# Kernel tuning notes

Measured on AMD Instinct MI355X. Metric: run time of the kernel, lower is better.

The kernel has to match this reference:

```python
import jax, jax.numpy as jnp
import numpy as np

IN_CH = 512
MAX_MID = 512


def setup_inputs() -> dict:
    key = jax.random.key(0)
    k0, k1, k2, k3, k4 = jax.random.split(key, 5)
    B, C, H, W = 32, IN_CH, 64, 64
    x = jax.random.normal(k0, (B, C, H, W), dtype=jnp.float32)
    # torch.nn.Linear params: weight [out, in], bias [out]
    s1 = 1.0 / np.sqrt(C)
    w1 = jax.random.uniform(k1, (MAX_MID * 2, C), minval=-s1, maxval=s1, dtype=jnp.float32)
    b1 = jax.random.uniform(k2, (MAX_MID * 2,), minval=-s1, maxval=s1, dtype=jnp.float32)
    s2 = 1.0 / np.sqrt(MAX_MID * 2)
    w2 = jax.random.uniform(k3, (MAX_MID, MAX_MID * 2), minval=-s2, maxval=s2, dtype=jnp.float32)
    b2 = jax.random.uniform(k4, (MAX_MID,), minval=-s2, maxval=s2, dtype=jnp.float32)
    return {"x": x, "w1": w1, "b1": b1, "w2": w2, "b2": b2}


def reference(x, w1, b1, w2, b2):
    # Global average pool: [B, C, H, W] -> [B, C]
    gap = jnp.mean(x, axis=(2, 3))
    # Tiny 2-layer MLP: Linear -> ReLU -> Linear -> Sigmoid
    h = jax.nn.relu(gap @ w1.T + b1)
    scores = jax.nn.sigmoid(h @ w2.T + b2)  # [B, MAX_MID]
    B, M = scores.shape
    # Eval path: scale from mean score, clamped
    scale = jnp.clip(jnp.mean(scores), 0.25, 1.0)
    k_min = max(4, M // 4)
    k = jnp.clip(jnp.ceil(M * scale).astype(jnp.int32), k_min, M)  # scalar int
    # topk mask with dynamic k but static shapes: threshold = k-th largest per row
    sorted_desc = jnp.sort(scores, axis=1)[:, ::-1]  # [B, M] descending
    idx = jnp.full((B, 1), k - 1, dtype=jnp.int32)
    thresh = jnp.take_along_axis(sorted_desc, idx, axis=1)  # [B, 1]
    mask = (scores >= thresh).astype(scores.dtype)  # [B, M]
    return mask[:, :, None, None], k
```

## Files before the change

### kernel.cpp

```cpp
#include <hip/hip_runtime.h>

#define NB    32
#define CIN   512
#define MID2  1024
#define MID   512
#define HW    4096

typedef float f32x4 __attribute__((ext_vector_type(4)));

__global__ __launch_bounds__(256, 8) void k_gap(const float* __restrict__ x,
                                                float* __restrict__ gap) {
    const int r0 = blockIdx.x * 2;
    const int t  = threadIdx.x;
    const f32x4* p0 = (const f32x4*)(x + (size_t)r0 * HW);
    const f32x4* p1 = (const f32x4*)(x + (size_t)(r0 + 1) * HW);
    float a0 = 0.f, a1 = 0.f;
#pragma unroll
    for (int i = 0; i < 4; ++i) {
        f32x4 u = __builtin_nontemporal_load(&p0[i * 256 + t]);
        f32x4 v = __builtin_nontemporal_load(&p1[i * 256 + t]);
        a0 += (u.x + u.y) + (u.z + u.w);
        a1 += (v.x + v.y) + (v.z + v.w);
    }
    for (int off = 32; off; off >>= 1) {
        a0 += __shfl_down(a0, off, 64);
        a1 += __shfl_down(a1, off, 64);
    }
    __shared__ float w0[4], w1[4];
    const int wid = t >> 6, lane = t & 63;
    if (lane == 0) { w0[wid] = a0; w1[wid] = a1; }
    __syncthreads();
    if (t == 0) gap[r0]     = ((w0[0] + w0[1]) + (w0[2] + w0[3])) * (1.0f / HW);
    if (t == 1) gap[r0 + 1] = ((w1[0] + w1[1]) + (w1[2] + w1[3])) * (1.0f / HW);
}

__global__ __launch_bounds__(256) void k_fc1(const float* __restrict__ gap,
                                             const float* __restrict__ w1,
                                             const float* __restrict__ b1,
                                             float* __restrict__ h) {
    const int wid = threadIdx.x >> 6, lane = threadIdx.x & 63;
    const int o4 = (blockIdx.x * 4 + wid) * 4;
    const int b  = o4 >> 10;
    const int j0 = o4 & (MID2 - 1);
    const float* g = gap + b * CIN + lane * 8;
    const float4 g0 = *(const float4*)g;
    const float4 g1 = *(const float4*)(g + 4);
    float s[4];
#pragma unroll
    for (int r = 0; r < 4; ++r) {
        const float* w = w1 + (size_t)(j0 + r) * CIN + lane * 8;
        const float4 a = *(const float4*)w;
        const float4 c = *(const float4*)(w + 4);
        s[r] = (a.x * g0.x + a.y * g0.y) + (a.z * g0.z + a.w * g0.w) +
               (c.x * g1.x + c.y * g1.y) + (c.z * g1.z + c.w * g1.w);
    }
#pragma unroll
    for (int r = 0; r < 4; ++r)
        for (int off = 32; off; off >>= 1) s[r] += __shfl_down(s[r], off, 64);
    if (lane == 0) {
#pragma unroll
        for (int r = 0; r < 4; ++r) h[o4 + r] = fmaxf(s[r] + b1[j0 + r], 0.f);
    }
}

__global__ __launch_bounds__(256) void k_fc2(const float* __restrict__ h,
                                             const float* __restrict__ w2,
                                             const float* __restrict__ b2,
                                             float* __restrict__ scores) {
    const int wid = threadIdx.x >> 6, lane = threadIdx.x & 63;
    const int o4 = (blockIdx.x * 4 + wid) * 4;
    const int b  = o4 >> 9;
    const int m0 = o4 & (MID - 1);
    const float4* h4 = (const float4*)(h + b * MID2 + lane * 16);
    const float4 h0 = h4[0], h1 = h4[1], h2 = h4[2], h3 = h4[3];
    float s[4];
#pragma unroll
    for (int r = 0; r < 4; ++r) {
        const float4* w = (const float4*)(w2 + (size_t)(m0 + r) * MID2 + lane * 16);
        const float4 a = w[0], c = w[1], d = w[2], e = w[3];
        s[r] = (a.x * h0.x + a.y * h0.y) + (a.z * h0.z + a.w * h0.w) +
               (c.x * h1.x + c.y * h1.y) + (c.z * h1.z + c.w * h1.w) +
               (d.x * h2.x + d.y * h2.y) + (d.z * h2.z + d.w * h2.w) +
               (e.x * h3.x + e.y * h3.y) + (e.z * h3.z + e.w * h3.w);
    }
#pragma unroll
    for (int r = 0; r < 4; ++r)
        for (int off = 32; off; off >>= 1) s[r] += __shfl_down(s[r], off, 64);
    if (lane == 0) {
#pragma unroll
        for (int r = 0; r < 4; ++r) {
            const float v = s[r] + b2[m0 + r];
            scores[o4 + r] = 1.0f / (1.0f + __expf(-v));
        }
    }
}

__global__ __launch_bounds__(512) void k_mask(const float* __restrict__ scores,
                                              float* __restrict__ out) {
    __shared__ float srow[MID];
    __shared__ float red[8];
    __shared__ float thr;
    const int b = blockIdx.x, t = threadIdx.x;

    float s = 0.f;
#pragma unroll
    for (int i = 0; i < NB * MID / 512; ++i) s += scores[i * 512 + t];
    for (int off = 32; off; off >>= 1) s += __shfl_down(s, off, 64);
    const int wid = t >> 6, lane = t & 63;
    if (lane == 0) red[wid] = s;

    const float v = scores[b * MID + t];
    srow[t] = v;
    __syncthreads();

    const float tot = ((red[0] + red[1]) + (red[2] + red[3])) +
                      ((red[4] + red[5]) + (red[6] + red[7]));
    const float mean = tot / (float)(NB * MID);
    const float scale = fminf(fmaxf(mean, 0.25f), 1.0f);
    int k = (int)ceilf((float)MID * scale);
    k = min(max(k, 128), MID);

    const float4* srow4 = (const float4*)srow;
    int gt = 0, ge = 0;
    for (int i = 0; i < MID / 4; ++i) {
        const float4 u = srow4[i];
        gt += (u.x > v) + (u.y > v) + (u.z > v) + (u.w > v);
        ge += (u.x >= v) + (u.y >= v) + (u.z >= v) + (u.w >= v);
    }
    if (gt < k && ge >= k) thr = v;
    __syncthreads();
    out[b * MID + t] = (v >= thr) ? 1.0f : 0.0f;
    if (b == 0 && t == 0) out[NB * MID] = (float)k;
}

extern "C" void kernel_launch(void* const* d_in, const int* in_sizes, int n_in,
                              void* d_out, int out_size, void* d_ws, size_t ws_size,
                              hipStream_t stream) {
    const float* x  = (const float*)d_in[0];
    const float* w1 = (const float*)d_in[1];
    const float* b1 = (const float*)d_in[2];
    const float* w2 = (const float*)d_in[3];
    const float* b2 = (const float*)d_in[4];
    float* out = (float*)d_out;

    float* gap    = (float*)d_ws;
    float* h      = gap + NB * CIN;
    float* scores = h + NB * MID2;

    k_gap <<<NB * CIN / 2,       256, 0, stream>>>(x, gap);
    k_fc1 <<<NB * MID2 / (4*4),  256, 0, stream>>>(gap, w1, b1, h);
    k_fc2 <<<NB * MID  / (4*4),  256, 0, stream>>>(h, w2, b2, scores);
    k_mask<<<NB,                 512, 0, stream>>>(scores, out);
}
```

Before: 67.33 us.

## Fuse GAP, two FC layers and top-k mask into one cooperative kernel

Replaces the four separate launches with a single cooperative kernel of 512 blocks that uses grid-wide syncs between the pooling, FC1, FC2 and mask phases. Each warp now pools 8 rows and computes more outputs per FC phase. This removes kernel launch gaps and tail effects, but the pooling phase, which streams a 256 MB input and dominates the work, now runs on fewer resident waves (512 blocks, launch bounds of 4 blocks per CU), which may lower memory-level parallelism. Host attribute and occupancy queries are added on every call, and the old four-kernel path is kept as a fallback.

```diff
diff --git a/kernel.cpp b/kernel.cpp
--- a/kernel.cpp
+++ b/kernel.cpp
@@ -1,4 +1,7 @@
 #include <hip/hip_runtime.h>
+#include <hip/hip_cooperative_groups.h>
+
+namespace cg = cooperative_groups;
 
 #define NB    32
 #define CIN   512
@@ -6,7 +9,141 @@
 #define MID   512
 #define HW    4096
 
+#define NBLK  512
+
 typedef float f32x4 __attribute__((ext_vector_type(4)));
+
+__global__ __launch_bounds__(256, 4) void k_all(const float* __restrict__ x,
+                                                const float* __restrict__ w1,
+                                                const float* __restrict__ b1,
+                                                const float* __restrict__ w2,
+                                                const float* __restrict__ b2,
+                                                float* __restrict__ out,
+                                                float* __restrict__ gap,
+                                                float* __restrict__ h,
+                                                float* __restrict__ scores) {
+    cg::grid_group grid = cg::this_grid();
+    const int wid = threadIdx.x >> 6, lane = threadIdx.x & 63;
+    const int wId = blockIdx.x * 4 + wid;
+
+#pragma unroll 1
+    for (int rr = 0; rr < 8; ++rr) {
+        const int row = wId * 8 + rr;
+        const f32x4* p = (const f32x4*)(x + (size_t)row * HW);
+        float s0 = 0.f, s1 = 0.f, s2 = 0.f, s3 = 0.f;
+#pragma unroll
+        for (int i = 0; i < 4; ++i) {
+            f32x4 a = __builtin_nontemporal_load(&p[(4 * i + 0) * 64 + lane]);
+            f32x4 b = __builtin_nontemporal_load(&p[(4 * i + 1) * 64 + lane]);
+            f32x4 c = __builtin_nontemporal_load(&p[(4 * i + 2) * 64 + lane]);
+            f32x4 d = __builtin_nontemporal_load(&p[(4 * i + 3) * 64 + lane]);
+            s0 += (a.x + a.y) + (a.z + a.w);
+            s1 += (b.x + b.y) + (b.z + b.w);
+            s2 += (c.x + c.y) + (c.z + c.w);
+            s3 += (d.x + d.y) + (d.z + d.w);
+        }
+        float s = (s0 + s1) + (s2 + s3);
+        for (int off = 32; off; off >>= 1) s += __shfl_down(s, off, 64);
+        if (lane == 0) gap[row] = s * (1.0f / HW);
+    }
+    grid.sync();
+
+    {
+        const int o0 = wId * 16;
+        const int b  = o0 >> 10;
+        const int j0 = o0 & (MID2 - 1);
+        const float* g = gap + b * CIN + lane * 8;
+        const float4 g0 = *(const float4*)g;
+        const float4 g1 = *(const float4*)(g + 4);
+        float s[16];
+#pragma unroll
+        for (int r = 0; r < 16; ++r) {
+            const float* w = w1 + (size_t)(j0 + r) * CIN + lane * 8;
+            const float4 a = *(const float4*)w;
+            const float4 c = *(const float4*)(w + 4);
+            s[r] = (a.x * g0.x + a.y * g0.y) + (a.z * g0.z + a.w * g0.w) +
+                   (c.x * g1.x + c.y * g1.y) + (c.z * g1.z + c.w * g1.w);
+        }
+#pragma unroll
+        for (int r = 0; r < 16; ++r)
+            for (int off = 32; off; off >>= 1) s[r] += __shfl_down(s[r], off, 64);
+        if (lane == 0) {
+#pragma unroll
+            for (int r = 0; r < 16; ++r) h[o0 + r] = fmaxf(s[r] + b1[j0 + r], 0.f);
+        }
+    }
+    grid.sync();
+
+    {
+        const int o0 = wId * 8;
+        const int b  = o0 >> 9;
+        const int m0 = o0 & (MID - 1);
+        const float4* h4 = (const float4*)(h + b * MID2 + lane * 16);
+        const float4 h0 = h4[0], h1 = h4[1], h2 = h4[2], h3 = h4[3];
+        float s[8];
+#pragma unroll
+        for (int r = 0; r < 8; ++r) {
+            const float4* w = (const float4*)(w2 + (size_t)(m0 + r) * MID2 + lane * 16);
+            const float4 a = w[0], c = w[1], d = w[2], e = w[3];
+            s[r] = (a.x * h0.x + a.y * h0.y) + (a.z * h0.z + a.w * h0.w) +
+                   (c.x * h1.x + c.y * h1.y) + (c.z * h1.z + c.w * h1.w) +
+                   (d.x * h2.x + d.y * h2.y) + (d.z * h2.z + d.w * h2.w) +
+                   (e.x * h3.x + e.y * h3.y) + (e.z * h3.z + e.w * h3.w);
+        }
+#pragma unroll
+        for (int r = 0; r < 8; ++r)
+            for (int off = 32; off; off >>= 1) s[r] += __shfl_down(s[r], off, 64);
+        if (lane == 0) {
+#pragma unroll
+            for (int r = 0; r < 8; ++r) {
+                const float v = s[r] + b2[m0 + r];
+                scores[o0 + r] = 1.0f / (1.0f + __expf(-v));
+            }
+        }
+    }
+    grid.sync();
+
+    const int b = blockIdx.x;
+    if (b >= NB) return;
+    const int t = threadIdx.x;
+    __shared__ float srow[MID];
+    __shared__ float red[4];
+    __shared__ float thr;
+
+    float s = 0.f;
+#pragma unroll
+    for (int i = 0; i < NB * MID / 256; ++i) s += scores[i * 256 + t];
+    for (int off = 32; off; off >>= 1) s += __shfl_down(s, off, 64);
+    if (lane == 0) red[wid] = s;
+
+    const float v0 = scores[b * MID + t];
+    const float v1 = scores[b * MID + t + 256];
+    srow[t]       = v0;
+    srow[t + 256] = v1;
+    __syncthreads();
+
+    const float tot = (red[0] + red[1]) + (red[2] + red[3]);
+    const float mean = tot / (float)(NB * MID);
+    const float scale = fminf(fmaxf(mean, 0.25f), 1.0f);
+    int k = (int)ceilf((float)MID * scale);
+    k = min(max(k, 128), MID);
+
+    const float4* srow4 = (const float4*)srow;
+    int gt0 = 0, ge0 = 0, gt1 = 0, ge1 = 0;
+    for (int i = 0; i < MID / 4; ++i) {
+        const float4 u = srow4[i];
+        gt0 += (u.x > v0) + (u.y > v0) + (u.z > v0) + (u.w > v0);
+        ge0 += (u.x >= v0) + (u.y >= v0) + (u.z >= v0) + (u.w >= v0);
+        gt1 += (u.x > v1) + (u.y > v1) + (u.z > v1) + (u.w > v1);
+        ge1 += (u.x >= v1) + (u.y >= v1) + (u.z >= v1) + (u.w >= v1);
+    }
+    if (gt0 < k && ge0 >= k) thr = v0;
+    if (gt1 < k && ge1 >= k) thr = v1;
+    __syncthreads();
+    out[b * MID + t]       = (v0 >= thr) ? 1.0f : 0.0f;
+    out[b * MID + t + 256] = (v1 >= thr) ? 1.0f : 0.0f;
+    if (b == 0 && t == 0) out[NB * MID] = (float)k;
+}
 
 __global__ __launch_bounds__(256, 8) void k_gap(const float* __restrict__ x,
                                                 float* __restrict__ gap) {
@@ -147,8 +284,24 @@
     float* h      = gap + NB * CIN;
     float* scores = h + NB * MID2;
 
-    k_gap <<<NB * CIN / 2,       256, 0, stream>>>(x, gap);
-    k_fc1 <<<NB * MID2 / (4*4),  256, 0, stream>>>(gap, w1, b1, h);
-    k_fc2 <<<NB * MID  / (4*4),  256, 0, stream>>>(h, w2, b2, scores);
-    k_mask<<<NB,                 512, 0, stream>>>(scores, out);
-}
+    int dev = 0;
+    hipGetDevice(&dev);
+    int coop = 0, ncu = 0, maxb = 0;
+    hipDeviceGetAttribute(&coop, hipDeviceAttributeCooperativeLaunch, dev);
+    hipDeviceGetAttribute(&ncu, hipDeviceAttributeMultiprocessorCount, dev);
+    hipOccupancyMaxActiveBlocksPerMultiprocessor(&maxb, (const void*)k_all, 256, 0);
+
+    hipError_t ret = hipErrorUnknown;
+    if (coop && (long)maxb * ncu >= NBLK) {
+        void* args[] = { (void*)&x, (void*)&w1, (void*)&b1, (void*)&w2, (void*)&b2,
+                         (void*)&out, (void*)&gap, (void*)&h, (void*)&scores };
+        ret = hipLaunchCooperativeKernel((const void*)k_all, dim3(NBLK), dim3(256),
+                                         args, 0, stream);
+    }
+    if (ret != hipSuccess) {
+        k_gap <<<NB * CIN / 2,      256, 0, stream>>>(x, gap);
+        k_fc1 <<<NB * MID2 / (4*4), 256, 0, stream>>>(gap, w1, b1, h);
+        k_fc2 <<<NB * MID  / (4*4), 256, 0, stream>>>(h, w2, b2, scores);
+        k_mask<<<NB,                512, 0, stream>>>(scores, out);
+    }
+}
```

Result: slower. 236.7 us (+251.6%).

## Fuse fc1, fc2 and mask kernels into one persistent kernel with grid barriers

Applied to the files above, without the earlier changes.

Merges the three small MLP and mask kernels into a single 512-block kernel that uses atomic-counter grid barriers between stages, with counters reset by the pooling kernel. Each wave now computes more outputs per stage, and the mask stage runs with 256 threads handling two elements each. This removes two kernel launch gaps, but adds spin-wait barrier latency and relies on all 512 blocks being co-resident to avoid deadlock.

```diff
diff --git a/kernel.cpp b/kernel.cpp
--- a/kernel.cpp
+++ b/kernel.cpp
@@ -6,10 +6,13 @@
 #define MID   512
 #define HW    4096
 
+#define MLPB  512
+
 typedef float f32x4 __attribute__((ext_vector_type(4)));
 
 __global__ __launch_bounds__(256, 8) void k_gap(const float* __restrict__ x,
-                                                float* __restrict__ gap) {
+                                                float* __restrict__ gap,
+                                                unsigned int* cnt) {
     const int r0 = blockIdx.x * 2;
     const int t  = threadIdx.x;
     const f32x4* p0 = (const f32x4*)(x + (size_t)r0 * HW);
@@ -32,104 +35,143 @@
     __syncthreads();
     if (t == 0) gap[r0]     = ((w0[0] + w0[1]) + (w0[2] + w0[3])) * (1.0f / HW);
     if (t == 1) gap[r0 + 1] = ((w1[0] + w1[1]) + (w1[2] + w1[3])) * (1.0f / HW);
+    if (blockIdx.x == 0 && t == 2) { cnt[0] = 0u; cnt[1] = 0u; }
 }
 
-__global__ __launch_bounds__(256) void k_fc1(const float* __restrict__ gap,
-                                             const float* __restrict__ w1,
-                                             const float* __restrict__ b1,
-                                             float* __restrict__ h) {
-    const int wid = threadIdx.x >> 6, lane = threadIdx.x & 63;
-    const int o4 = (blockIdx.x * 4 + wid) * 4;
-    const int b  = o4 >> 10;
-    const int j0 = o4 & (MID2 - 1);
-    const float* g = gap + b * CIN + lane * 8;
-    const float4 g0 = *(const float4*)g;
-    const float4 g1 = *(const float4*)(g + 4);
-    float s[4];
-#pragma unroll
-    for (int r = 0; r < 4; ++r) {
-        const float* w = w1 + (size_t)(j0 + r) * CIN + lane * 8;
-        const float4 a = *(const float4*)w;
-        const float4 c = *(const float4*)(w + 4);
-        s[r] = (a.x * g0.x + a.y * g0.y) + (a.z * g0.z + a.w * g0.w) +
-               (c.x * g1.x + c.y * g1.y) + (c.z * g1.z + c.w * g1.w);
+__device__ __forceinline__ void barrier_arrive(unsigned int* c) {
+    __threadfence();
+    __syncthreads();
+    if (threadIdx.x == 0)
+        __hip_atomic_fetch_add(c, 1u, __ATOMIC_RELEASE, __HIP_MEMORY_SCOPE_AGENT);
+}
+__device__ __forceinline__ void barrier_wait(unsigned int* c) {
+    if (threadIdx.x == 0) {
+        while (__hip_atomic_load(c, __ATOMIC_ACQUIRE, __HIP_MEMORY_SCOPE_AGENT)
+               < (unsigned)MLPB) {
+            __builtin_amdgcn_s_sleep(8);
+        }
     }
-#pragma unroll
-    for (int r = 0; r < 4; ++r)
-        for (int off = 32; off; off >>= 1) s[r] += __shfl_down(s[r], off, 64);
-    if (lane == 0) {
-#pragma unroll
-        for (int r = 0; r < 4; ++r) h[o4 + r] = fmaxf(s[r] + b1[j0 + r], 0.f);
-    }
+    __syncthreads();
+    __threadfence();
 }
 
-__global__ __launch_bounds__(256) void k_fc2(const float* __restrict__ h,
-                                             const float* __restrict__ w2,
-                                             const float* __restrict__ b2,
-                                             float* __restrict__ scores) {
-    const int wid = threadIdx.x >> 6, lane = threadIdx.x & 63;
-    const int o4 = (blockIdx.x * 4 + wid) * 4;
-    const int b  = o4 >> 9;
-    const int m0 = o4 & (MID - 1);
-    const float4* h4 = (const float4*)(h + b * MID2 + lane * 16);
-    const float4 h0 = h4[0], h1 = h4[1], h2 = h4[2], h3 = h4[3];
-    float s[4];
+__global__ __launch_bounds__(256, 8) void k_mlp(const float* __restrict__ gap,
+                                                const float* __restrict__ w1,
+                                                const float* __restrict__ b1,
+                                                const float* __restrict__ w2,
+                                                const float* __restrict__ b2,
+                                                float* h,
+                                                float* scores,
+                                                float* out,
+                                                unsigned int* cnt) {
+    const int t = threadIdx.x, wid = t >> 6, lane = t & 63;
+    const int gwave = blockIdx.x * 4 + wid;
+
+    {
+        const int o0 = gwave * 16;
+        const int b  = o0 >> 10;
+        const int j0 = o0 & (MID2 - 1);
+        const float* g = gap + b * CIN + lane * 8;
+        const float4 g0 = *(const float4*)g;
+        const float4 g1 = *(const float4*)(g + 4);
 #pragma unroll
-    for (int r = 0; r < 4; ++r) {
-        const float4* w = (const float4*)(w2 + (size_t)(m0 + r) * MID2 + lane * 16);
-        const float4 a = w[0], c = w[1], d = w[2], e = w[3];
-        s[r] = (a.x * h0.x + a.y * h0.y) + (a.z * h0.z + a.w * h0.w) +
-               (c.x * h1.x + c.y * h1.y) + (c.z * h1.z + c.w * h1.w) +
-               (d.x * h2.x + d.y * h2.y) + (d.z * h2.z + d.w * h2.w) +
-               (e.x * h3.x + e.y * h3.y) + (e.z * h3.z + e.w * h3.w);
-    }
+        for (int grp = 0; grp < 4; ++grp) {
+            float s[4];
 #pragma unroll
-    for (int r = 0; r < 4; ++r)
-        for (int off = 32; off; off >>= 1) s[r] += __shfl_down(s[r], off, 64);
-    if (lane == 0) {
+            for (int r = 0; r < 4; ++r) {
+                const float* w = w1 + (size_t)(j0 + grp * 4 + r) * CIN + lane * 8;
+                const float4 a = *(const float4*)w;
+                const float4 c = *(const float4*)(w + 4);
+                s[r] = (a.x * g0.x + a.y * g0.y) + (a.z * g0.z + a.w * g0.w) +
+                       (c.x * g1.x + c.y * g1.y) + (c.z * g1.z + c.w * g1.w);
+            }
 #pragma unroll
-        for (int r = 0; r < 4; ++r) {
-            const float v = s[r] + b2[m0 + r];
-            scores[o4 + r] = 1.0f / (1.0f + __expf(-v));
+            for (int r = 0; r < 4; ++r)
+                for (int off = 32; off; off >>= 1) s[r] += __shfl_down(s[r], off, 64);
+            if (lane == 0) {
+#pragma unroll
+                for (int r = 0; r < 4; ++r) {
+                    const int j = j0 + grp * 4 + r;
+                    h[o0 + grp * 4 + r] = fmaxf(s[r] + b1[j], 0.f);
+                }
+            }
         }
     }
-}
+    barrier_arrive(&cnt[0]);
+    barrier_wait(&cnt[0]);
 
-__global__ __launch_bounds__(512) void k_mask(const float* __restrict__ scores,
-                                              float* __restrict__ out) {
+    {
+        const int o0 = gwave * 8;
+        const int b  = o0 >> 9;
+        const int m0 = o0 & (MID - 1);
+        const float4* h4 = (const float4*)(h + b * MID2 + lane * 16);
+        const float4 h0 = h4[0], h1 = h4[1], h2 = h4[2], h3 = h4[3];
+#pragma unroll
+        for (int grp = 0; grp < 2; ++grp) {
+            float s[4];
+#pragma unroll
+            for (int r = 0; r < 4; ++r) {
+                const float4* w = (const float4*)(w2 + (size_t)(m0 + grp * 4 + r) * MID2 + lane * 16);
+                const float4 a = w[0], c = w[1], d = w[2], e = w[3];
+                s[r] = (a.x * h0.x + a.y * h0.y) + (a.z * h0.z + a.w * h0.w) +
+                       (c.x * h1.x + c.y * h1.y) + (c.z * h1.z + c.w * h1.w) +
+                       (d.x * h2.x + d.y * h2.y) + (d.z * h2.z + d.w * h2.w) +
+                       (e.x * h3.x + e.y * h3.y) + (e.z * h3.z + e.w * h3.w);
+            }
+#pragma unroll
+            for (int r = 0; r < 4; ++r)
+                for (int off = 32; off; off >>= 1) s[r] += __shfl_down(s[r], off, 64);
+            if (lane == 0) {
+#pragma unroll
+                for (int r = 0; r < 4; ++r) {
+                    const int m = o0 + grp * 4 + r;
+                    const float v = s[r] + b2[m0 + grp * 4 + r];
+                    scores[m] = 1.0f / (1.0f + __expf(-v));
+                }
+            }
+        }
+    }
+    barrier_arrive(&cnt[1]);
+    if (blockIdx.x >= NB) return;
+    barrier_wait(&cnt[1]);
+
+    const int b = blockIdx.x;
     __shared__ float srow[MID];
-    __shared__ float red[8];
+    __shared__ float red[4];
     __shared__ float thr;
-    const int b = blockIdx.x, t = threadIdx.x;
 
     float s = 0.f;
 #pragma unroll
-    for (int i = 0; i < NB * MID / 512; ++i) s += scores[i * 512 + t];
+    for (int i = 0; i < NB * MID / 256; ++i) s += scores[i * 256 + t];
     for (int off = 32; off; off >>= 1) s += __shfl_down(s, off, 64);
-    const int wid = t >> 6, lane = t & 63;
     if (lane == 0) red[wid] = s;
 
-    const float v = scores[b * MID + t];
-    srow[t] = v;
+    const float v0 = scores[b * MID + t];
+    const float v1 = scores[b * MID + t + 256];
+    srow[t]       = v0;
+    srow[t + 256] = v1;
     __syncthreads();
 
-    const float tot = ((red[0] + red[1]) + (red[2] + red[3])) +
-                      ((red[4] + red[5]) + (red[6] + red[7]));
+    const float tot = (red[0] + red[1]) + (red[2] + red[3]);
     const float mean = tot / (float)(NB * MID);
     const float scale = fminf(fmaxf(mean, 0.25f), 1.0f);
     int k = (int)ceilf((float)MID * scale);
     k = min(max(k, 128), MID);
 
     const float4* srow4 = (const float4*)srow;
-    int gt = 0, ge = 0;
+    int gt0 = 0, ge0 = 0, gt1 = 0, ge1 = 0;
     for (int i = 0; i < MID / 4; ++i) {
         const float4 u = srow4[i];
-        gt += (u.x > v) + (u.y > v) + (u.z > v) + (u.w > v);
-        ge += (u.x >= v) + (u.y >= v) + (u.z >= v) + (u.w >= v);
+        gt0 += (u.x > v0) + (u.y > v0) + (u.z > v0) + (u.w > v0);
+        ge0 += (u.x >= v0) + (u.y >= v0) + (u.z >= v0) + (u.w >= v0);
+        gt1 += (u.x > v1) + (u.y > v1) + (u.z > v1) + (u.w > v1);
+        ge1 += (u.x >= v1) + (u.y >= v1) + (u.z >= v1) + (u.w >= v1);
     }
-    if (gt < k && ge >= k) thr = v;
+    if (gt0 < k && ge0 >= k) thr = v0;
+    if (gt1 < k && ge1 >= k) thr = v1;
     __syncthreads();
-    out[b * MID + t] = (v >= thr) ? 1.0f : 0.0f;
+    out[b * MID + t]       = (v0 >= thr) ? 1.0f : 0.0f;
+    out[b * MID + t + 256] = (v1 >= thr) ? 1.0f : 0.0f;
     if (b == 0 && t == 0) out[NB * MID] = (float)k;
 }
 
@@ -146,9 +188,8 @@
     float* gap    = (float*)d_ws;
     float* h      = gap + NB * CIN;
     float* scores = h + NB * MID2;
+    unsigned int* cnt = (unsigned int*)(scores + NB * MID);
 
-    k_gap <<<NB * CIN / 2,       256, 0, stream>>>(x, gap);
-    k_fc1 <<<NB * MID2 / (4*4),  256, 0, stream>>>(gap, w1, b1, h);
-    k_fc2 <<<NB * MID  / (4*4),  256, 0, stream>>>(h, w2, b2, scores);
-    k_mask<<<NB,                 512, 0, stream>>>(scores, out);
+    k_gap<<<NB * CIN / 2, 256, 0, stream>>>(x, gap, cnt);
+    k_mlp<<<MLPB,         256, 0, stream>>>(gap, w1, b1, w2, b2, h, scores, out, cnt);
 }
```

New measurement: 225.3 us. +234.6%, slower.
